# Optimization experiments

Measured on AMD Instinct MI355X. Metric: run time of the kernel, lower is better.

Reference implementation:

```python
import jax, jax.numpy as jnp
import numpy as np

N, K, M = 4096, 128, 512  # conformers, dihedrals, atoms


def setup_inputs() -> dict:
    key = jax.random.key(0)
    k1, k2 = jax.random.split(key)
    inp = jax.random.normal(k1, (N, K), dtype=jnp.float32)          # target dihedral deltas (rad)
    pos0 = jax.random.normal(k2, (N, M, 3), dtype=jnp.float32)      # initial conformer coordinates
    base = jnp.arange(K, dtype=jnp.int32)
    # chain molecule: dihedral k defined by atoms (k, k+1, k+2, k+3)
    angles = jnp.stack([base, base + 1, base + 2, base + 3], axis=1)  # (K, 4)
    # rdkit toBeMovedIdxList on a chain for bond (k+1, k+2): atoms k+3 .. M-1 move
    move_mask = jnp.arange(M)[None, :] > (base + 2)[:, None]          # (K, M) bool
    return {"input": inp, "pos0": pos0, "angles": angles, "move_mask": move_mask}


def _rot_matrix(theta, axis):
    # rdkit Transform3D::SetRotation: R = (1-cos)*aa^T + [[c,-sZ,sY],[sZ,c,-sX],[-sY,sX,c]]
    cosT = jnp.cos(theta)
    sinT = jnp.sin(theta)
    t = 1.0 - cosT
    outer = t[:, None, None] * axis[:, :, None] * axis[:, None, :]   # (N,3,3)
    X, Y, Z = axis[:, 0], axis[:, 1], axis[:, 2]
    mat1 = jnp.stack(
        [cosT, -sinT * Z, sinT * Y,
         sinT * Z, cosT, -sinT * X,
         -sinT * Y, sinT * X, cosT], axis=1
    ).reshape(-1, 3, 3)
    return outer + mat1


def _step(pos, x):
    ang, mask, theta = x                       # (4,), (M,), (N,)
    p = jnp.take(pos, ang, axis=1)             # (N,4,3) gather of i,j,k,l atoms
    rIJ = p[:, 1] - p[:, 0]
    rJK = p[:, 2] - p[:, 1]
    rKL = p[:, 3] - p[:, 2]
    nIJK = jnp.cross(rIJ, rJK)
    nJKL = jnp.cross(rJK, rKL)
    m = jnp.cross(nIJK, rJK)
    nrm = lambda v: jnp.linalg.norm(v, axis=-1)
    sin_arg = jnp.sum(m * nJKL, axis=-1) / (nrm(nJKL) * nrm(m))
    cos_arg = jnp.sum(nIJK * nJKL, axis=-1) / (nrm(nIJK) * nrm(nJKL))
    values = theta + jnp.arctan2(sin_arg, cos_arg)   # rotation angle per conformer
    begin = p[:, 1]                                   # rotation axis origin (atom j)
    d = p[:, 2] - p[:, 1]
    # torch.nn.functional.normalize with eps=1e-12
    axis = d / jnp.maximum(jnp.linalg.norm(d, axis=-1, keepdims=True), 1e-12)
    R = _rot_matrix(values, axis)                     # (N,3,3)
    rotated = jnp.einsum('nij,nmj->nmi', R, pos - begin[:, None, :]) + begin[:, None, :]
    pos = jnp.where(mask[None, :, None], rotated, pos)
    return pos, None


def reference(input, pos0, angles, move_mask):
    xs = (angles, move_mask, input.T)                 # scan over K dihedrals (sequential recurrence)
    pos, _ = jax.lax.scan(_step, pos0, xs)
    return pos
```

## Files before the change

kernel.cpp:

```cpp
#include <hip/hip_runtime.h>


#define NK 128
#define NM 512
#define NMOL 4096
#define TPB 128

#define COMPOSE_QP()                                                     \
    do {                                                                 \
        float n00=q00*p00+q01*p10+q02*p20;                               \
        float n01=q00*p01+q01*p11+q02*p21;                               \
        float n02=q00*p02+q01*p12+q02*p22;                               \
        float n10=q10*p00+q11*p10+q12*p20;                               \
        float n11=q10*p01+q11*p11+q12*p21;                               \
        float n12=q10*p02+q11*p12+q12*p22;                               \
        float n20=q20*p00+q21*p10+q22*p20;                               \
        float n21=q20*p01+q21*p11+q22*p21;                               \
        float n22=q20*p02+q21*p12+q22*p22;                               \
        float ntx=q00*ptx+q01*pty+q02*ptz+qtx;                           \
        float nty=q10*ptx+q11*pty+q12*ptz+qty;                           \
        float ntz=q20*ptx+q21*pty+q22*ptz+qtz;                           \
        p00=n00;p01=n01;p02=n02;p10=n10;p11=n11;p12=n12;                 \
        p20=n20;p21=n21;p22=n22;ptx=ntx;pty=nty;ptz=ntz;                 \
    } while (0)

__global__ __launch_bounds__(TPB) void dihedral_scan_kernel(
    const float* __restrict__ theta,
    const float* __restrict__ pos0,
    float* __restrict__ out)
{
    const int tid = threadIdx.x;
    const int mol = blockIdx.x;
    const float* __restrict__ pb = pos0 + (size_t)mol * (NM * 3);
    float*       __restrict__ ob = out  + (size_t)mol * (NM * 3);

    __shared__ float sA[(NK + 3) * 3];
    __shared__ float sT[12];
    __shared__ float sF[12];

    for (int i = tid; i < (NK + 3) * 3; i += TPB) sA[i] = pb[i];
    const float th = theta[(size_t)mol * NK + tid];
    __syncthreads();

    const float* ap = &sA[tid * 3];
    const float a0x = ap[0], a0y = ap[1],  a0z = ap[2];
    const float a1x = ap[3], a1y = ap[4],  a1z = ap[5];
    const float a2x = ap[6], a2y = ap[7],  a2z = ap[8];
    const float a3x = ap[9], a3y = ap[10], a3z = ap[11];

    const float ijx = a1x - a0x, ijy = a1y - a0y, ijz = a1z - a0z;
    const float jkx = a2x - a1x, jky = a2y - a1y, jkz = a2z - a1z;
    const float klx = a3x - a2x, kly = a3y - a2y, klz = a3z - a2z;
    const float n1x = ijy*jkz - ijz*jky, n1y = ijz*jkx - ijx*jkz, n1z = ijx*jky - ijy*jkx;
    const float n2x = jky*klz - jkz*kly, n2y = jkz*klx - jkx*klz, n2z = jkx*kly - jky*klx;
    const float mx  = n1y*jkz - n1z*jky, my  = n1z*jkx - n1x*jkz, mz  = n1x*jky - n1y*jkx;
    const float dmn = mx*n2x + my*n2y + mz*n2z;
    const float dnn = n1x*n2x + n1y*n2y + n1z*n2z;
    const float Lm  = mx*mx + my*my + mz*mz;
    const float L1  = n1x*n1x + n1y*n1y + n1z*n1z;
    const float L2  = n2x*n2x + n2y*n2y + n2z*n2z;

    float sphi = dmn * rsqrtf(Lm * L2);
    float cphi = dnn * rsqrtf(L1 * L2);
    const float rn = rsqrtf(sphi * sphi + cphi * cphi);
    sphi *= rn; cphi *= rn;
    float sth, cth;
    sincosf(th, &sth, &cth);
    const float c = cth * cphi - sth * sphi;
    const float s = sth * cphi + cth * sphi;

    const float Ljk  = jkx*jkx + jky*jky + jkz*jkz;
    const float inva = rsqrtf(fmaxf(Ljk, 1e-24f));
    const float ax = jkx * inva, ay = jky * inva, az = jkz * inva;

    const float t1 = 1.0f - c;
    float p00 = t1*ax*ax + c,    p01 = t1*ax*ay - s*az, p02 = t1*ax*az + s*ay;
    float p10 = t1*ay*ax + s*az, p11 = t1*ay*ay + c,    p12 = t1*ay*az - s*ax;
    float p20 = t1*az*ax - s*ay, p21 = t1*az*ay + s*ax, p22 = t1*az*az + c;
    float ptx = a1x - (p00*a1x + p01*a1y + p02*a1z);
    float pty = a1y - (p10*a1x + p11*a1y + p12*a1z);
    float ptz = a1z - (p20*a1x + p21*a1y + p22*a1z);

    const int lane = tid & 63;
    #pragma unroll
    for (int off = 1; off < 64; off <<= 1) {
        const float q00 = __shfl_up(p00, off, 64), q01 = __shfl_up(p01, off, 64), q02 = __shfl_up(p02, off, 64);
        const float q10 = __shfl_up(p10, off, 64), q11 = __shfl_up(p11, off, 64), q12 = __shfl_up(p12, off, 64);
        const float q20 = __shfl_up(p20, off, 64), q21 = __shfl_up(p21, off, 64), q22 = __shfl_up(p22, off, 64);
        const float qtx = __shfl_up(ptx, off, 64), qty = __shfl_up(pty, off, 64), qtz = __shfl_up(ptz, off, 64);
        if (lane >= off) { COMPOSE_QP(); }
    }
    if (tid == 63) {
        sT[0]=p00; sT[1]=p01; sT[2]=p02; sT[3]=p10; sT[4]=p11; sT[5]=p12;
        sT[6]=p20; sT[7]=p21; sT[8]=p22; sT[9]=ptx; sT[10]=pty; sT[11]=ptz;
    }
    __syncthreads();
    if (tid >= 64) {
        const float q00=sT[0], q01=sT[1], q02=sT[2];
        const float q10=sT[3], q11=sT[4], q12=sT[5];
        const float q20=sT[6], q21=sT[7], q22=sT[8];
        const float qtx=sT[9], qty=sT[10], qtz=sT[11];
        COMPOSE_QP();
    }

    {
        const float ox = p00*a3x + p01*a3y + p02*a3z + ptx;
        const float oy = p10*a3x + p11*a3y + p12*a3z + pty;
        const float oz = p20*a3x + p21*a3y + p22*a3z + ptz;
        float* op = ob + (size_t)(tid + 3) * 3;
        op[0] = ox; op[1] = oy; op[2] = oz;
    }
    if (tid < 9) ob[tid] = sA[tid];
    if (tid == 127) {
        sF[0]=p00; sF[1]=p01; sF[2]=p02; sF[3]=p10; sF[4]=p11; sF[5]=p12;
        sF[6]=p20; sF[7]=p21; sF[8]=p22; sF[9]=ptx; sF[10]=pty; sF[11]=ptz;
    }
    __syncthreads();

    const float f00=sF[0], f01=sF[1], f02=sF[2];
    const float f10=sF[3], f11=sF[4], f12=sF[5];
    const float f20=sF[6], f21=sF[7], f22=sF[8];
    const float ftx=sF[9], fty=sF[10], ftz=sF[11];
    for (int mi = NK + 3 + tid; mi < NM; mi += TPB) {
        const float x = pb[mi*3 + 0], y = pb[mi*3 + 1], z = pb[mi*3 + 2];
        float* op = ob + (size_t)mi * 3;
        op[0] = f00*x + f01*y + f02*z + ftx;
        op[1] = f10*x + f11*y + f12*z + fty;
        op[2] = f20*x + f21*y + f22*z + ftz;
    }
}

extern "C" void kernel_launch(void* const* d_in, const int* in_sizes, int n_in,
                              void* d_out, int out_size, void* d_ws, size_t ws_size,
                              hipStream_t stream) {
    const float* theta = (const float*)d_in[0];
    const float* pos0  = (const float*)d_in[1];
    float* out = (float*)d_out;
    dihedral_scan_kernel<<<NMOL, TPB, 0, stream>>>(theta, pos0, out);
}
```

Measured before the change: 19.57 us.

## Use quaternion scan with one wavefront per molecule and vectorized IO

Rigid transforms are now stored as quaternion plus translation (7 floats instead of 12), so each step of the wavefront prefix scan shuffles and composes less data. Each wavefront handles one molecule, with each lane covering two dihedrals, which removes the cross-wave shared-memory handoff and one barrier. Loads and stores now use float4 and are staged through shared memory, and tail atoms are prefetched into registers before the scan. The half-angle quaternion is built with sqrt/copysign, which may shift rounding relative to the matrix form.

```diff
diff --git a/kernel.cpp b/kernel.cpp
--- a/kernel.cpp
+++ b/kernel.cpp
@@ -4,130 +4,177 @@
 #define NK 128
 #define NM 512
 #define NMOL 4096
-#define TPB 128
+#define TPB 256
+#define MPB 4
 
-#define COMPOSE_QP()                                                     \
-    do {                                                                 \
-        float n00=q00*p00+q01*p10+q02*p20;                               \
-        float n01=q00*p01+q01*p11+q02*p21;                               \
-        float n02=q00*p02+q01*p12+q02*p22;                               \
-        float n10=q10*p00+q11*p10+q12*p20;                               \
-        float n11=q10*p01+q11*p11+q12*p21;                               \
-        float n12=q10*p02+q11*p12+q12*p22;                               \
-        float n20=q20*p00+q21*p10+q22*p20;                               \
-        float n21=q20*p01+q21*p11+q22*p21;                               \
-        float n22=q20*p02+q21*p12+q22*p22;                               \
-        float ntx=q00*ptx+q01*pty+q02*ptz+qtx;                           \
-        float nty=q10*ptx+q11*pty+q12*ptz+qty;                           \
-        float ntz=q20*ptx+q21*pty+q22*ptz+qtz;                           \
-        p00=n00;p01=n01;p02=n02;p10=n10;p11=n11;p12=n12;                 \
-        p20=n20;p21=n21;p22=n22;ptx=ntx;pty=nty;ptz=ntz;                 \
-    } while (0)
+struct Aff { float qw, qx, qy, qz, tx, ty, tz; };
 
-__global__ __launch_bounds__(TPB) void dihedral_scan_kernel(
+__device__ __forceinline__ void qrot(float qw, float qx, float qy, float qz,
+                                     float vx, float vy, float vz,
+                                     float& ox, float& oy, float& oz) {
+    const float ux = qy*vz - qz*vy + qw*vx;
+    const float uy = qz*vx - qx*vz + qw*vy;
+    const float uz = qx*vy - qy*vx + qw*vz;
+    ox = vx + 2.f*(qy*uz - qz*uy);
+    oy = vy + 2.f*(qz*ux - qx*uz);
+    oz = vz + 2.f*(qx*uy - qy*ux);
+}
+
+__device__ __forceinline__ Aff aff_compose(const Aff& Q, const Aff& P) {
+    Aff r;
+    r.qw = Q.qw*P.qw - Q.qx*P.qx - Q.qy*P.qy - Q.qz*P.qz;
+    r.qx = Q.qw*P.qx + Q.qx*P.qw + Q.qy*P.qz - Q.qz*P.qy;
+    r.qy = Q.qw*P.qy - Q.qx*P.qz + Q.qy*P.qw + Q.qz*P.qx;
+    r.qz = Q.qw*P.qz + Q.qx*P.qy - Q.qy*P.qx + Q.qz*P.qw;
+    float rx, ry, rz;
+    qrot(Q.qw, Q.qx, Q.qy, Q.qz, P.tx, P.ty, P.tz, rx, ry, rz);
+    r.tx = rx + Q.tx; r.ty = ry + Q.ty; r.tz = rz + Q.tz;
+    return r;
+}
+
+__device__ __forceinline__ void qnorm(Aff& a) {
+    const float r = rsqrtf(a.qw*a.qw + a.qx*a.qx + a.qy*a.qy + a.qz*a.qz);
+    a.qw *= r; a.qx *= r; a.qy *= r; a.qz *= r;
+}
+
+__device__ __forceinline__ Aff build_B(const float* a, float th) {
+    const float ijx=a[3]-a[0], ijy=a[4]-a[1],  ijz=a[5]-a[2];
+    const float jkx=a[6]-a[3], jky=a[7]-a[4],  jkz=a[8]-a[5];
+    const float klx=a[9]-a[6], kly=a[10]-a[7], klz=a[11]-a[8];
+    const float n1x=ijy*jkz-ijz*jky, n1y=ijz*jkx-ijx*jkz, n1z=ijx*jky-ijy*jkx;
+    const float n2x=jky*klz-jkz*kly, n2y=jkz*klx-jkx*klz, n2z=jkx*kly-jky*klx;
+    const float mx =n1y*jkz-n1z*jky, my =n1z*jkx-n1x*jkz, mz =n1x*jky-n1y*jkx;
+    const float dmn=mx*n2x+my*n2y+mz*n2z;
+    const float dnn=n1x*n2x+n1y*n2y+n1z*n2z;
+    const float Lm =mx*mx+my*my+mz*mz;
+    const float L1 =n1x*n1x+n1y*n1y+n1z*n1z;
+    const float L2 =n2x*n2x+n2y*n2y+n2z*n2z;
+    float sphi = dmn*rsqrtf(Lm*L2);
+    float cphi = dnn*rsqrtf(L1*L2);
+    const float rn = rsqrtf(sphi*sphi + cphi*cphi);
+    sphi *= rn; cphi *= rn;
+    float sth, cth; sincosf(th, &sth, &cth);
+    const float c = cth*cphi - sth*sphi;
+    const float s = sth*cphi + cth*sphi;
+    const float Ljk = jkx*jkx + jky*jky + jkz*jkz;
+    const float inva = rsqrtf(fmaxf(Ljk, 1e-24f));
+    const float ax = jkx*inva, ay = jky*inva, az = jkz*inva;
+    const float hc = sqrtf(fmaxf(0.f, 0.5f*(1.f + c)));
+    const float hs = copysignf(sqrtf(fmaxf(0.f, 0.5f*(1.f - c))), s);
+    Aff b;
+    b.qw = hc; b.qx = hs*ax; b.qy = hs*ay; b.qz = hs*az;
+    float rx, ry, rz;
+    qrot(b.qw, b.qx, b.qy, b.qz, a[3], a[4], a[5], rx, ry, rz);
+    b.tx = a[3] - rx; b.ty = a[4] - ry; b.tz = a[5] - rz;
+    return b;
+}
+
+#define SHFL_AFF_UP(D, S, off)                                           \
+    D.qw = __shfl_up(S.qw, off, 64); D.qx = __shfl_up(S.qx, off, 64);    \
+    D.qy = __shfl_up(S.qy, off, 64); D.qz = __shfl_up(S.qz, off, 64);    \
+    D.tx = __shfl_up(S.tx, off, 64); D.ty = __shfl_up(S.ty, off, 64);    \
+    D.tz = __shfl_up(S.tz, off, 64);
+
+__global__ __launch_bounds__(TPB, 4) void dihedral_quat_scan_kernel(
     const float* __restrict__ theta,
     const float* __restrict__ pos0,
     float* __restrict__ out)
 {
-    const int tid = threadIdx.x;
-    const int mol = blockIdx.x;
-    const float* __restrict__ pb = pos0 + (size_t)mol * (NM * 3);
-    float*       __restrict__ ob = out  + (size_t)mol * (NM * 3);
+    const int tid  = threadIdx.x;
+    const int lane = tid & 63;
+    const int wid  = tid >> 6;
+    const int mol  = blockIdx.x * MPB + wid;
+    const float4* __restrict__ pb4 = (const float4*)(pos0 + (size_t)mol * (NM*3));
+    float4*       __restrict__ ob4 = (float4*)(out  + (size_t)mol * (NM*3));
 
-    __shared__ float sA[(NK + 3) * 3];
-    __shared__ float sT[12];
-    __shared__ float sF[12];
+    __shared__ float sA[MPB][400];
+    __shared__ float sO[MPB][400];
 
-    for (int i = tid; i < (NK + 3) * 3; i += TPB) sA[i] = pb[i];
-    const float th = theta[(size_t)mol * NK + tid];
+    float4* sA4 = (float4*)sA[wid];
+    for (int i = lane; i < 99; i += 64) sA4[i] = pb4[i];
+    const float2 th2 = ((const float2*)(theta + (size_t)mol * NK))[lane];
+
+    const int t0 = lane, t1 = 64 + lane;
+    const bool has2 = (t1 < 95);
+    float4 Ta0, Ta1, Ta2, Tb0, Tb1, Tb2;
+    { const int b = 99 + 3*t0; Ta0 = pb4[b]; Ta1 = pb4[b+1]; Ta2 = pb4[b+2]; }
+    if (has2) { const int b = 99 + 3*t1; Tb0 = pb4[b]; Tb1 = pb4[b+1]; Tb2 = pb4[b+2]; }
+
     __syncthreads();
 
-    const float* ap = &sA[tid * 3];
-    const float a0x = ap[0], a0y = ap[1],  a0z = ap[2];
-    const float a1x = ap[3], a1y = ap[4],  a1z = ap[5];
-    const float a2x = ap[6], a2y = ap[7],  a2z = ap[8];
-    const float a3x = ap[9], a3y = ap[10], a3z = ap[11];
+    float A[15];
+    const float* ap = &sA[wid][lane * 6];
+    #pragma unroll
+    for (int i = 0; i < 15; ++i) A[i] = ap[i];
 
-    const float ijx = a1x - a0x, ijy = a1y - a0y, ijz = a1z - a0z;
-    const float jkx = a2x - a1x, jky = a2y - a1y, jkz = a2z - a1z;
-    const float klx = a3x - a2x, kly = a3y - a2y, klz = a3z - a2z;
-    const float n1x = ijy*jkz - ijz*jky, n1y = ijz*jkx - ijx*jkz, n1z = ijx*jky - ijy*jkx;
-    const float n2x = jky*klz - jkz*kly, n2y = jkz*klx - jkx*klz, n2z = jkx*kly - jky*klx;
-    const float mx  = n1y*jkz - n1z*jky, my  = n1z*jkx - n1x*jkz, mz  = n1x*jky - n1y*jkx;
-    const float dmn = mx*n2x + my*n2y + mz*n2z;
-    const float dnn = n1x*n2x + n1y*n2y + n1z*n2z;
-    const float Lm  = mx*mx + my*my + mz*mz;
-    const float L1  = n1x*n1x + n1y*n1y + n1z*n1z;
-    const float L2  = n2x*n2x + n2y*n2y + n2z*n2z;
+    Aff Bev = build_B(&A[0], th2.x);
+    Aff Bod = build_B(&A[3], th2.y);
+    Aff S   = aff_compose(Bev, Bod);
 
-    float sphi = dmn * rsqrtf(Lm * L2);
-    float cphi = dnn * rsqrtf(L1 * L2);
-    const float rn = rsqrtf(sphi * sphi + cphi * cphi);
-    sphi *= rn; cphi *= rn;
-    float sth, cth;
-    sincosf(th, &sth, &cth);
-    const float c = cth * cphi - sth * sphi;
-    const float s = sth * cphi + cth * sphi;
-
-    const float Ljk  = jkx*jkx + jky*jky + jkz*jkz;
-    const float inva = rsqrtf(fmaxf(Ljk, 1e-24f));
-    const float ax = jkx * inva, ay = jky * inva, az = jkz * inva;
-
-    const float t1 = 1.0f - c;
-    float p00 = t1*ax*ax + c,    p01 = t1*ax*ay - s*az, p02 = t1*ax*az + s*ay;
-    float p10 = t1*ay*ax + s*az, p11 = t1*ay*ay + c,    p12 = t1*ay*az - s*ax;
-    float p20 = t1*az*ax - s*ay, p21 = t1*az*ay + s*ax, p22 = t1*az*az + c;
-    float ptx = a1x - (p00*a1x + p01*a1y + p02*a1z);
-    float pty = a1y - (p10*a1x + p11*a1y + p12*a1z);
-    float ptz = a1z - (p20*a1x + p21*a1y + p22*a1z);
-
-    const int lane = tid & 63;
     #pragma unroll
     for (int off = 1; off < 64; off <<= 1) {
-        const float q00 = __shfl_up(p00, off, 64), q01 = __shfl_up(p01, off, 64), q02 = __shfl_up(p02, off, 64);
-        const float q10 = __shfl_up(p10, off, 64), q11 = __shfl_up(p11, off, 64), q12 = __shfl_up(p12, off, 64);
-        const float q20 = __shfl_up(p20, off, 64), q21 = __shfl_up(p21, off, 64), q22 = __shfl_up(p22, off, 64);
-        const float qtx = __shfl_up(ptx, off, 64), qty = __shfl_up(pty, off, 64), qtz = __shfl_up(ptz, off, 64);
-        if (lane >= off) { COMPOSE_QP(); }
+        Aff Q; SHFL_AFF_UP(Q, S, off);
+        if (lane >= off) S = aff_compose(Q, S);
     }
-    if (tid == 63) {
-        sT[0]=p00; sT[1]=p01; sT[2]=p02; sT[3]=p10; sT[4]=p11; sT[5]=p12;
-        sT[6]=p20; sT[7]=p21; sT[8]=p22; sT[9]=ptx; sT[10]=pty; sT[11]=ptz;
+    Aff E; SHFL_AFF_UP(E, S, 1);
+    if (lane == 0) { E.qw = 1.f; E.qx = E.qy = E.qz = 0.f; E.tx = E.ty = E.tz = 0.f; }
+    Aff Pe = aff_compose(E, Bev);
+    qnorm(Pe); qnorm(S);
+
+    {
+        float ox, oy, oz;
+        float* op = &sO[wid][lane * 6 + 9];
+        qrot(Pe.qw, Pe.qx, Pe.qy, Pe.qz, A[9], A[10], A[11], ox, oy, oz);
+        op[0] = ox + Pe.tx; op[1] = oy + Pe.ty; op[2] = oz + Pe.tz;
+        qrot(S.qw, S.qx, S.qy, S.qz, A[12], A[13], A[14], ox, oy, oz);
+        op[3] = ox + S.tx;  op[4] = oy + S.ty;  op[5] = oz + S.tz;
     }
-    __syncthreads();
-    if (tid >= 64) {
-        const float q00=sT[0], q01=sT[1], q02=sT[2];
-        const float q10=sT[3], q11=sT[4], q12=sT[5];
-        const float q20=sT[6], q21=sT[7], q22=sT[8];
-        const float qtx=sT[9], qty=sT[10], qtz=sT[11];
-        COMPOSE_QP();
+    if (lane < 9) sO[wid][lane] = sA[wid][lane];
+    if (lane == 63) {
+        float ox, oy, oz;
+        qrot(S.qw, S.qx, S.qy, S.qz, sA[wid][393], sA[wid][394], sA[wid][395], ox, oy, oz);
+        sO[wid][393] = ox + S.tx; sO[wid][394] = oy + S.ty; sO[wid][395] = oz + S.tz;
     }
 
-    {
-        const float ox = p00*a3x + p01*a3y + p02*a3z + ptx;
-        const float oy = p10*a3x + p11*a3y + p12*a3z + pty;
-        const float oz = p20*a3x + p21*a3y + p22*a3z + ptz;
-        float* op = ob + (size_t)(tid + 3) * 3;
-        op[0] = ox; op[1] = oy; op[2] = oz;
-    }
-    if (tid < 9) ob[tid] = sA[tid];
-    if (tid == 127) {
-        sF[0]=p00; sF[1]=p01; sF[2]=p02; sF[3]=p10; sF[4]=p11; sF[5]=p12;
-        sF[6]=p20; sF[7]=p21; sF[8]=p22; sF[9]=ptx; sF[10]=pty; sF[11]=ptz;
-    }
+    Aff F;
+    F.qw = __shfl(S.qw, 63, 64); F.qx = __shfl(S.qx, 63, 64);
+    F.qy = __shfl(S.qy, 63, 64); F.qz = __shfl(S.qz, 63, 64);
+    F.tx = __shfl(S.tx, 63, 64); F.ty = __shfl(S.ty, 63, 64);
+    F.tz = __shfl(S.tz, 63, 64);
+    const float f00 = 1.f - 2.f*(F.qy*F.qy + F.qz*F.qz);
+    const float f01 = 2.f*(F.qx*F.qy - F.qw*F.qz);
+    const float f02 = 2.f*(F.qx*F.qz + F.qw*F.qy);
+    const float f10 = 2.f*(F.qx*F.qy + F.qw*F.qz);
+    const float f11 = 1.f - 2.f*(F.qx*F.qx + F.qz*F.qz);
+    const float f12 = 2.f*(F.qy*F.qz - F.qw*F.qx);
+    const float f20 = 2.f*(F.qx*F.qz - F.qw*F.qy);
+    const float f21 = 2.f*(F.qy*F.qz + F.qw*F.qx);
+    const float f22 = 1.f - 2.f*(F.qx*F.qx + F.qy*F.qy);
+
     __syncthreads();
 
-    const float f00=sF[0], f01=sF[1], f02=sF[2];
-    const float f10=sF[3], f11=sF[4], f12=sF[5];
-    const float f20=sF[6], f21=sF[7], f22=sF[8];
-    const float ftx=sF[9], fty=sF[10], ftz=sF[11];
-    for (int mi = NK + 3 + tid; mi < NM; mi += TPB) {
-        const float x = pb[mi*3 + 0], y = pb[mi*3 + 1], z = pb[mi*3 + 2];
-        float* op = ob + (size_t)mi * 3;
-        op[0] = f00*x + f01*y + f02*z + ftx;
-        op[1] = f10*x + f11*y + f12*z + fty;
-        op[2] = f20*x + f21*y + f22*z + ftz;
-    }
+    const float4* sO4 = (const float4*)sO[wid];
+    for (int i = lane; i < 99; i += 64) ob4[i] = sO4[i];
+
+    #define TAIL_EMIT(b, va, vb, vc)                                          \
+    do {                                                                      \
+        const float x0=va.x, y0=va.y, z0=va.z;                                \
+        const float x1=va.w, y1=vb.x, z1=vb.y;                                \
+        const float x2=vb.z, y2=vb.w, z2=vc.x;                                \
+        const float x3=vc.y, y3=vc.z, z3=vc.w;                                \
+        float4 o0, o1, o2;                                                    \
+        o0.x = f00*x0+f01*y0+f02*z0+F.tx; o0.y = f10*x0+f11*y0+f12*z0+F.ty;   \
+        o0.z = f20*x0+f21*y0+f22*z0+F.tz; o0.w = f00*x1+f01*y1+f02*z1+F.tx;   \
+        o1.x = f10*x1+f11*y1+f12*z1+F.ty; o1.y = f20*x1+f21*y1+f22*z1+F.tz;   \
+        o1.z = f00*x2+f01*y2+f02*z2+F.tx; o1.w = f10*x2+f11*y2+f12*z2+F.ty;   \
+        o2.x = f20*x2+f21*y2+f22*z2+F.tz; o2.y = f00*x3+f01*y3+f02*z3+F.tx;   \
+        o2.z = f10*x3+f11*y3+f12*z3+F.ty; o2.w = f20*x3+f21*y3+f22*z3+F.tz;   \
+        ob4[(b)] = o0; ob4[(b)+1] = o1; ob4[(b)+2] = o2;                      \
+    } while (0)
+
+    TAIL_EMIT(99 + 3*t0, Ta0, Ta1, Ta2);
+    if (has2) TAIL_EMIT(99 + 3*t1, Tb0, Tb1, Tb2);
+    #undef TAIL_EMIT
 }
 
 extern "C" void kernel_launch(void* const* d_in, const int* in_sizes, int n_in,
@@ -136,5 +183,5 @@
     const float* theta = (const float*)d_in[0];
     const float* pos0  = (const float*)d_in[1];
     float* out = (float*)d_out;
-    dihedral_scan_kernel<<<NMOL, TPB, 0, stream>>>(theta, pos0, out);
+    dihedral_quat_scan_kernel<<<NMOL / MPB, TPB, 0, stream>>>(theta, pos0, out);
 }
```

New measurement: 19.08 us. 2.5% less time.
